# Performance work log

Hardware: AMD Instinct MI355X
Metric: run time of the kernel (lower is better)

The kernel has to match this reference:

```python
import jax, jax.numpy as jnp
import numpy as np

B, L, HIDDEN, HEAD_DIM = 8, 1024, 1024, 64


def setup_inputs() -> dict:
    key = jax.random.key(0)
    ks = jax.random.split(key, 11)
    s = 1.0 / np.sqrt(HIDDEN)
    return {
        "query": jax.random.normal(ks[0], (B, L, HIDDEN), jnp.float32),
        "key": jax.random.normal(ks[1], (B, L, HIDDEN), jnp.float32),
        "value": jax.random.normal(ks[2], (B, L, HIDDEN), jnp.float32),
        "k_bias_matrix": jax.random.normal(ks[3], (L, L, HEAD_DIM), jnp.float32) * 0.02,
        "v_bias_matrix": jax.random.normal(ks[4], (L, L, HEAD_DIM), jnp.float32) * 0.02,
        "Wq": jax.random.normal(ks[5], (HIDDEN, HEAD_DIM), jnp.float32) * s,
        "bq": jnp.zeros((HEAD_DIM,), jnp.float32),
        "Wk": jax.random.normal(ks[6], (HIDDEN, HEAD_DIM), jnp.float32) * s,
        "bk": jnp.zeros((HEAD_DIM,), jnp.float32),
        "Wv": jax.random.normal(ks[7], (HIDDEN, HEAD_DIM), jnp.float32) * s,
        "bv": jnp.zeros((HEAD_DIM,), jnp.float32),
        "mask": jnp.ones((B, L), jnp.int32),
    }


def reference(query, key, value, k_bias_matrix, v_bias_matrix, Wq, bq, Wk, bk, Wv, bv, mask):
    # projections to head_dim
    q = query @ Wq + bq  # [B,L,D]
    k = key @ Wk + bk    # [B,L,D]
    v = value @ Wv + bv  # [B,L,D]
    # content scores + relative key-bias scores (Shaw et al.)
    attn_1 = jnp.einsum('bqd,bkd->bqk', q, k)              # [B,L,L]
    attn_2 = jnp.einsum('bqd,qkd->bqk', q, k_bias_matrix)  # [B,L,L]
    scores = (attn_1 + attn_2) / jnp.sqrt(jnp.asarray(q.shape[-1], q.dtype))
    scores = jnp.where(mask[:, None, :] == 0, jnp.asarray(-1e9, scores.dtype), scores)
    w = jax.nn.softmax(scores, axis=-1)                    # [B,L,L]
    values_1 = jnp.einsum('bqk,bkd->bqd', w, v)
    values_2 = jnp.einsum('bqk,qkd->bqd', w, v_bias_matrix)
    return values_1 + values_2
```

## Files before the change

kernel.cpp:

```cpp
#include <hip/hip_runtime.h>

#define B_ 8
#define L_ 1024
#define HID_ 1024
#define D_ 64

typedef short bf16x8 __attribute__((ext_vector_type(8)));
typedef float f32x4 __attribute__((ext_vector_type(4)));

__device__ inline short f2bf(float f) {
    unsigned u = __builtin_bit_cast(unsigned, f);
    unsigned r = (u + 0x7fffu + ((u >> 16) & 1u)) >> 16;
    return (short)r;
}

__global__ __launch_bounds__(256) void proj_kernel(
    const float* __restrict__ query, const float* __restrict__ key, const float* __restrict__ value,
    const float* __restrict__ Wq, const float* __restrict__ bq,
    const float* __restrict__ Wk, const float* __restrict__ bk,
    const float* __restrict__ Wv, const float* __restrict__ bv,
    float* __restrict__ qp, float* __restrict__ kp, float* __restrict__ vp)
{
    const int which = blockIdx.y;
    const float* in   = which == 0 ? query : (which == 1 ? key : value);
    const float* W    = which == 0 ? Wq : (which == 1 ? Wk : Wv);
    const float* bias = which == 0 ? bq : (which == 1 ? bk : bv);
    float* out        = which == 0 ? qp : (which == 1 ? kp : vp);

    __shared__ float Xs[64][68];
    __shared__ float Ws[64][64];

    const int t  = threadIdx.x;
    const int tx = t & 15;
    const int ty = t >> 4;
    const int r0 = blockIdx.x * 64;

    float acc[4][4] = {};
    for (int kk = 0; kk < HID_; kk += 64) {
        {
            const int r  = t >> 4;
            const int c4 = t & 15;
            #pragma unroll
            for (int i = 0; i < 4; i++) {
                float4 x = *(const float4*)(in + (size_t)(r0 + r + 16 * i) * HID_ + kk + 4 * c4);
                *(float4*)(&Xs[r + 16 * i][4 * c4]) = x;
                float4 w = *(const float4*)(W + (size_t)(kk + r + 16 * i) * D_ + 4 * c4);
                *(float4*)(&Ws[r + 16 * i][4 * c4]) = w;
            }
        }
        __syncthreads();
        #pragma unroll 8
        for (int k = 0; k < 64; k++) {
            float4 b4 = *(const float4*)(&Ws[k][4 * tx]);
            #pragma unroll
            for (int i = 0; i < 4; i++) {
                float a = Xs[4 * ty + i][k];
                acc[i][0] += a * b4.x;
                acc[i][1] += a * b4.y;
                acc[i][2] += a * b4.z;
                acc[i][3] += a * b4.w;
            }
        }
        __syncthreads();
    }
    float4 bb = *(const float4*)(bias + 4 * tx);
    #pragma unroll
    for (int i = 0; i < 4; i++) {
        float4 o;
        o.x = acc[i][0] + bb.x; o.y = acc[i][1] + bb.y;
        o.z = acc[i][2] + bb.z; o.w = acc[i][3] + bb.w;
        *(float4*)(out + (size_t)(r0 + 4 * ty + i) * D_ + 4 * tx) = o;
    }
}

__global__ __launch_bounds__(256) void attn1_kernel(
    const float* __restrict__ qp, const float* __restrict__ kp,
    const int* __restrict__ mask, float* __restrict__ s1)
{
    const int b  = blockIdx.z;
    const int q0 = blockIdx.y * 128;
    const int k0 = blockIdx.x * 128;
    __shared__ float qs[128][68];
    __shared__ float ks[128][68];
    const int t = threadIdx.x;
    {
        const int row = t >> 4;
        const int c4  = t & 15;
        #pragma unroll
        for (int i = 0; i < 8; i++) {
            int r = row + 16 * i;
            *(float4*)&qs[r][c4 * 4] = *(const float4*)(qp + ((size_t)b * L_ + q0 + r) * D_ + c4 * 4);
            *(float4*)&ks[r][c4 * 4] = *(const float4*)(kp + ((size_t)b * L_ + k0 + r) * D_ + c4 * 4);
        }
    }
    __syncthreads();
    const int tx = t & 15, ty = t >> 4;
    float acc[8][8] = {};
    for (int d4 = 0; d4 < 16; d4++) {
        float4 qv[8], kv[8];
        #pragma unroll
        for (int i = 0; i < 8; i++) qv[i] = *(const float4*)&qs[ty + 16 * i][d4 * 4];
        #pragma unroll
        for (int j = 0; j < 8; j++) kv[j] = *(const float4*)&ks[tx + 16 * j][d4 * 4];
        #pragma unroll
        for (int i = 0; i < 8; i++)
            #pragma unroll
            for (int j = 0; j < 8; j++)
                acc[i][j] += qv[i].x * kv[j].x + qv[i].y * kv[j].y +
                             qv[i].z * kv[j].z + qv[i].w * kv[j].w;
    }
    #pragma unroll
    for (int j = 0; j < 8; j++) {
        int kg = k0 + tx + 16 * j;
        bool live = mask[b * L_ + kg] != 0;
        #pragma unroll
        for (int i = 0; i < 8; i++) {
            int qg = q0 + ty + 16 * i;
            s1[((size_t)b * L_ + qg) * L_ + kg] = live ? acc[i][j] * 0.125f : -1e9f;
        }
    }
}

#define KS_ 1032
__global__ __launch_bounds__(512) void row_kernel(
    const float* __restrict__ qp, const float* __restrict__ kb,
    const float* __restrict__ vb, float* __restrict__ s1w,
    float* __restrict__ out)
{
    __shared__ float sc[2 * 8 * KS_];
    __shared__ short qbf[2 * 16 * 64];
    const int t = threadIdx.x;
    const int wave = t >> 6, lane = t & 63;
    const int q0 = blockIdx.x * 2;

    #pragma unroll
    for (int i = 0; i < 4; i++) {
        int idx = t + 512 * i;
        int d = idx & 63, bq = idx >> 6;
        int b = bq & 15, q = bq >> 4;
        float v = (b < 8) ? 0.125f * qp[((size_t)b * L_ + q0 + q) * D_ + d] : 0.0f;
        qbf[idx] = f2bf(v);
    }
    __syncthreads();

    for (int job = wave; job < 128; job += 8) {
        int q = job >> 6, kt = job & 63;
        int k0 = kt * 16;
        const float* abase = kb + ((size_t)(q0 + q) * L_ + k0 + (lane & 15)) * D_ + (lane >> 4) * 8;
        f32x4 acc = {0.f, 0.f, 0.f, 0.f};
        #pragma unroll
        for (int h = 0; h < 2; h++) {
            float4 x0 = *(const float4*)(abase + h * 32);
            float4 x1 = *(const float4*)(abase + h * 32 + 4);
            bf16x8 a;
            a[0] = f2bf(x0.x); a[1] = f2bf(x0.y); a[2] = f2bf(x0.z); a[3] = f2bf(x0.w);
            a[4] = f2bf(x1.x); a[5] = f2bf(x1.y); a[6] = f2bf(x1.z); a[7] = f2bf(x1.w);
            bf16x8 bq = *(const bf16x8*)&qbf[(q * 16 + (lane & 15)) * 64 + h * 32 + (lane >> 4) * 8];
            acc = __builtin_amdgcn_mfma_f32_16x16x32_bf16(a, bq, acc, 0, 0, 0);
        }
        int b = lane & 15;
        if (b < 8) {
            float* dst = &sc[(q * 8 + b) * KS_ + k0 + (lane >> 4) * 4];
            dst[0] = acc[0]; dst[1] = acc[1]; dst[2] = acc[2]; dst[3] = acc[3];
        }
    }
    __syncthreads();

    #pragma unroll
    for (int i = 0; i < 8; i++) {
        int idx = t + 512 * i;
        int c4 = idx & 255;
        int row = idx >> 8;
        int b = row & 7, q = row >> 3;
        float4 s = *(const float4*)(s1w + ((size_t)b * L_ + q0 + q) * L_ + c4 * 4);
        float* dst = &sc[(q * 8 + b) * KS_ + c4 * 4];
        float4 cur = *(float4*)dst;
        cur.x += s.x; cur.y += s.y; cur.z += s.z; cur.w += s.w;
        *(float4*)dst = cur;
    }
    __syncthreads();

    for (int r = wave; r < 16; r += 8) {
        int q = r >> 3, b = r & 7;
        float* rowp = &sc[r * KS_];
        float* wrow = s1w + ((size_t)b * L_ + q0 + q) * L_;
        float4 x[4];
        float m = -1e30f;
        #pragma unroll
        for (int j = 0; j < 4; j++) {
            x[j] = *(const float4*)&rowp[lane * 4 + 256 * j];
            m = fmaxf(m, fmaxf(fmaxf(x[j].x, x[j].y), fmaxf(x[j].z, x[j].w)));
        }
        #pragma unroll
        for (int off = 32; off; off >>= 1) m = fmaxf(m, __shfl_xor(m, off));
        float s = 0.f;
        #pragma unroll
        for (int j = 0; j < 4; j++) {
            x[j].x = __expf(x[j].x - m); x[j].y = __expf(x[j].y - m);
            x[j].z = __expf(x[j].z - m); x[j].w = __expf(x[j].w - m);
            s += x[j].x + x[j].y + x[j].z + x[j].w;
        }
        #pragma unroll
        for (int off = 32; off; off >>= 1) s += __shfl_xor(s, off);
        float inv = 1.0f / s;
        #pragma unroll
        for (int j = 0; j < 4; j++) {
            x[j].x *= inv; x[j].y *= inv; x[j].z *= inv; x[j].w *= inv;
            *(float4*)&rowp[lane * 4 + 256 * j] = x[j];
            *(float4*)&wrow[lane * 4 + 256 * j] = x[j];
        }
    }
    __syncthreads();

    {
        const int q  = wave >> 2;
        const int kqi = wave & 3;
        const int kq = kqi * 256;
        const int kl = lane >> 4;
        const int d4 = lane & 15;
        float acc[8][4] = {};
        const float* vbbase = vb + ((size_t)(q0 + q) * L_ + kq + kl) * D_ + d4 * 4;
        #pragma unroll 4
        for (int j = 0; j < 64; j++) {
            int k = kq + j * 4 + kl;
            float4 vb4 = *(const float4*)(vbbase + (size_t)j * 4 * D_);
            #pragma unroll
            for (int b = 0; b < 8; b++) {
                float wgt = sc[(q * 8 + b) * KS_ + k];
                acc[b][0] += wgt * vb4.x;
                acc[b][1] += wgt * vb4.y;
                acc[b][2] += wgt * vb4.z;
                acc[b][3] += wgt * vb4.w;
            }
        }
        #pragma unroll
        for (int b = 0; b < 8; b++)
            #pragma unroll
            for (int j = 0; j < 4; j++) {
                float v = acc[b][j];
                v += __shfl_down(v, 32);
                v += __shfl_down(v, 16);
                acc[b][j] = v;
            }
        __syncthreads();
        float* part = sc;
        if (lane < 16) {
            #pragma unroll
            for (int b = 0; b < 8; b++) {
                float4 o; o.x = acc[b][0]; o.y = acc[b][1]; o.z = acc[b][2]; o.w = acc[b][3];
                *(float4*)&part[(((q * 4 + kqi) * 8) + b) * 64 + d4 * 4] = o;
            }
        }
        __syncthreads();
        for (int i = t; i < 1024; i += 512) {
            int d = i & 63; int bq = i >> 6; int b = bq & 7; int q2 = bq >> 3;
            float s = part[((q2 * 4 + 0) * 8 + b) * 64 + d] +
                      part[((q2 * 4 + 1) * 8 + b) * 64 + d] +
                      part[((q2 * 4 + 2) * 8 + b) * 64 + d] +
                      part[((q2 * 4 + 3) * 8 + b) * 64 + d];
            out[((size_t)b * L_ + q0 + q2) * D_ + d] = s;
        }
    }
}

__global__ __launch_bounds__(256) void pv_kernel(
    const float* __restrict__ w, const float* __restrict__ vp, float* __restrict__ out)
{
    const int b  = blockIdx.y;
    const int q0 = blockIdx.x * 16;
    __shared__ float ws_[16][68];
    __shared__ float vs[64][64];
    const int t  = threadIdx.x;
    const int tx = t & 15;
    const int ty = t >> 4;
    float acc[4] = {};
    for (int kk = 0; kk < L_; kk += 64) {
        {
            int qi = t >> 4, kc = t & 15;
            float4 x = *(const float4*)(w + ((size_t)b * L_ + q0 + qi) * L_ + kk + 4 * kc);
            *(float4*)(&ws_[qi][4 * kc]) = x;
        }
        #pragma unroll
        for (int i = 0; i < 4; i++) {
            int f4 = t + 256 * i;
            int kr = f4 >> 4, dc = f4 & 15;
            float4 x = *(const float4*)(vp + ((size_t)b * L_ + kk + kr) * D_ + 4 * dc);
            *(float4*)(&vs[kr][4 * dc]) = x;
        }
        __syncthreads();
        #pragma unroll 8
        for (int k = 0; k < 64; k++) {
            float4 v4 = *(const float4*)(&vs[k][4 * tx]);
            float a = ws_[ty][k];
            acc[0] += a * v4.x; acc[1] += a * v4.y;
            acc[2] += a * v4.z; acc[3] += a * v4.w;
        }
        __syncthreads();
    }
    float* dst = out + ((size_t)b * L_ + q0 + ty) * D_ + 4 * tx;
    float4 o = *(const float4*)dst;
    o.x += acc[0]; o.y += acc[1]; o.z += acc[2]; o.w += acc[3];
    *(float4*)dst = o;
}

extern "C" void kernel_launch(void* const* d_in, const int* in_sizes, int n_in,
                              void* d_out, int out_size, void* d_ws, size_t ws_size,
                              hipStream_t stream)
{
    const float* query = (const float*)d_in[0];
    const float* key   = (const float*)d_in[1];
    const float* value = (const float*)d_in[2];
    const float* kb    = (const float*)d_in[3];
    const float* vb    = (const float*)d_in[4];
    const float* Wq    = (const float*)d_in[5];
    const float* bq    = (const float*)d_in[6];
    const float* Wk    = (const float*)d_in[7];
    const float* bk    = (const float*)d_in[8];
    const float* Wv    = (const float*)d_in[9];
    const float* bv    = (const float*)d_in[10];
    const int*   mask  = (const int*)d_in[11];
    float* out = (float*)d_out;

    float* ws = (float*)d_ws;
    const size_t PROJ = (size_t)B_ * L_ * D_;
    float* qp = ws;
    float* kp = ws + PROJ;
    float* vp = ws + 2 * PROJ;
    float* s1 = ws + 3 * PROJ;

    proj_kernel<<<dim3(128, 3), 256, 0, stream>>>(query, key, value,
                                                  Wq, bq, Wk, bk, Wv, bv,
                                                  qp, kp, vp);
    attn1_kernel<<<dim3(8, 8, 8), 256, 0, stream>>>(qp, kp, mask, s1);
    row_kernel<<<512, 512, 0, stream>>>(qp, kb, vb, s1, out);
    pv_kernel<<<dim3(64, 8), 256, 0, stream>>>(s1, vp, out);
}
```

Measured before the change: 690.4 us.

## Move QKV projection onto bf16 MFMA with split hi/lo precision

Replaces the fp32 shared-memory FMA projection with MFMA 16x16x32 bf16 instructions. Each fp32 activation is split into bf16 hi and lo parts, and three MFMAs per tile approximate fp32 accuracy. The weights are pre-split and pre-swizzled into MFMA fragment layout by a new small kernel that runs every call. This drops the LDS staging and syncs in exchange for an extra launch and some per-element conversion work.

New measurement: 684.9 us. No clear change (-0.8%).

```diff
diff --git a/kernel.cpp b/kernel.cpp
--- a/kernel.cpp
+++ b/kernel.cpp
@@ -13,63 +13,87 @@
     unsigned r = (u + 0x7fffu + ((u >> 16) & 1u)) >> 16;
     return (short)r;
 }
+__device__ inline float bf2f(short h) {
+    unsigned u = ((unsigned)(unsigned short)h) << 16;
+    return __builtin_bit_cast(float, u);
+}
+
+__global__ __launch_bounds__(256) void wconv_kernel(
+    const float* __restrict__ Wq, const float* __restrict__ Wk, const float* __restrict__ Wv,
+    unsigned short* __restrict__ whi, unsigned short* __restrict__ wlo)
+{
+    int t = blockIdx.x * 256 + threadIdx.x;
+    int which = t >> 16;
+    int rem = t & 65535;
+    int j = rem & 7, lane = (rem >> 3) & 63, ks = (rem >> 9) & 31, n = rem >> 14;
+    int k = ks * 32 + (lane >> 4) * 8 + j;
+    int d = n * 16 + (lane & 15);
+    const float* W = which == 0 ? Wq : (which == 1 ? Wk : Wv);
+    float v = W[k * D_ + d];
+    short h = f2bf(v);
+    whi[t] = (unsigned short)h;
+    wlo[t] = (unsigned short)f2bf(v - bf2f(h));
+}
 
 __global__ __launch_bounds__(256) void proj_kernel(
     const float* __restrict__ query, const float* __restrict__ key, const float* __restrict__ value,
-    const float* __restrict__ Wq, const float* __restrict__ bq,
-    const float* __restrict__ Wk, const float* __restrict__ bk,
-    const float* __restrict__ Wv, const float* __restrict__ bv,
+    const float* __restrict__ bq, const float* __restrict__ bk, const float* __restrict__ bv,
+    const unsigned short* __restrict__ whi, const unsigned short* __restrict__ wlo,
     float* __restrict__ qp, float* __restrict__ kp, float* __restrict__ vp)
 {
-    const int which = blockIdx.y;
+    const int blk = blockIdx.x;
+    const int which = blk >> 7;
+    const int r0 = (blk & 127) * 64;
     const float* in   = which == 0 ? query : (which == 1 ? key : value);
-    const float* W    = which == 0 ? Wq : (which == 1 ? Wk : Wv);
     const float* bias = which == 0 ? bq : (which == 1 ? bk : bv);
     float* out        = which == 0 ? qp : (which == 1 ? kp : vp);
-
-    __shared__ float Xs[64][68];
-    __shared__ float Ws[64][64];
-
-    const int t  = threadIdx.x;
-    const int tx = t & 15;
-    const int ty = t >> 4;
-    const int r0 = blockIdx.x * 64;
-
-    float acc[4][4] = {};
-    for (int kk = 0; kk < HID_; kk += 64) {
+    const unsigned short* wh = whi + (size_t)which * 65536;
+    const unsigned short* wl = wlo + (size_t)which * 65536;
+
+    const int wave = threadIdx.x >> 6, lane = threadIdx.x & 63;
+    const int lr = lane & 15, lg = lane >> 4;
+
+    const float* arow = in + (size_t)(r0 + wave * 16 + lr) * HID_ + lg * 8;
+
+    f32x4 acc[4];
+    #pragma unroll
+    for (int n = 0; n < 4; n++) acc[n] = (f32x4){0.f, 0.f, 0.f, 0.f};
+
+    #pragma unroll 2
+    for (int ks = 0; ks < 32; ks++) {
+        float4 x0 = *(const float4*)(arow + ks * 32);
+        float4 x1 = *(const float4*)(arow + ks * 32 + 4);
+        bf16x8 ahi, alo;
         {
-            const int r  = t >> 4;
-            const int c4 = t & 15;
-            #pragma unroll
-            for (int i = 0; i < 4; i++) {
-                float4 x = *(const float4*)(in + (size_t)(r0 + r + 16 * i) * HID_ + kk + 4 * c4);
-                *(float4*)(&Xs[r + 16 * i][4 * c4]) = x;
-                float4 w = *(const float4*)(W + (size_t)(kk + r + 16 * i) * D_ + 4 * c4);
-                *(float4*)(&Ws[r + 16 * i][4 * c4]) = w;
-            }
-        }
-        __syncthreads();
-        #pragma unroll 8
-        for (int k = 0; k < 64; k++) {
-            float4 b4 = *(const float4*)(&Ws[k][4 * tx]);
-            #pragma unroll
-            for (int i = 0; i < 4; i++) {
-                float a = Xs[4 * ty + i][k];
-                acc[i][0] += a * b4.x;
-                acc[i][1] += a * b4.y;
-                acc[i][2] += a * b4.z;
-                acc[i][3] += a * b4.w;
-            }
-        }
-        __syncthreads();
-    }
-    float4 bb = *(const float4*)(bias + 4 * tx);
-    #pragma unroll
-    for (int i = 0; i < 4; i++) {
-        float4 o;
-        o.x = acc[i][0] + bb.x; o.y = acc[i][1] + bb.y;
-        o.z = acc[i][2] + bb.z; o.w = acc[i][3] + bb.w;
-        *(float4*)(out + (size_t)(r0 + 4 * ty + i) * D_ + 4 * tx) = o;
+            float xs0 = x0.x, xs1 = x0.y, xs2 = x0.z, xs3 = x0.w;
+            float xs4 = x1.x, xs5 = x1.y, xs6 = x1.z, xs7 = x1.w;
+            short h;
+            h = f2bf(xs0); ahi[0] = h; alo[0] = f2bf(xs0 - bf2f(h));
+            h = f2bf(xs1); ahi[1] = h; alo[1] = f2bf(xs1 - bf2f(h));
+            h = f2bf(xs2); ahi[2] = h; alo[2] = f2bf(xs2 - bf2f(h));
+            h = f2bf(xs3); ahi[3] = h; alo[3] = f2bf(xs3 - bf2f(h));
+            h = f2bf(xs4); ahi[4] = h; alo[4] = f2bf(xs4 - bf2f(h));
+            h = f2bf(xs5); ahi[5] = h; alo[5] = f2bf(xs5 - bf2f(h));
+            h = f2bf(xs6); ahi[6] = h; alo[6] = f2bf(xs6 - bf2f(h));
+            h = f2bf(xs7); ahi[7] = h; alo[7] = f2bf(xs7 - bf2f(h));
+        }
+        #pragma unroll
+        for (int n = 0; n < 4; n++) {
+            const size_t fo = ((size_t)(n * 32 + ks) * 64 + lane) * 8;
+            bf16x8 bhi = *(const bf16x8*)(wh + fo);
+            bf16x8 blo = *(const bf16x8*)(wl + fo);
+            acc[n] = __builtin_amdgcn_mfma_f32_16x16x32_bf16(ahi, bhi, acc[n], 0, 0, 0);
+            acc[n] = __builtin_amdgcn_mfma_f32_16x16x32_bf16(alo, bhi, acc[n], 0, 0, 0);
+            acc[n] = __builtin_amdgcn_mfma_f32_16x16x32_bf16(ahi, blo, acc[n], 0, 0, 0);
+        }
+    }
+    #pragma unroll
+    for (int n = 0; n < 4; n++) {
+        float bv_ = bias[n * 16 + lr];
+        #pragma unroll
+        for (int i = 0; i < 4; i++) {
+            out[(size_t)(r0 + wave * 16 + lg * 4 + i) * D_ + n * 16 + lr] = acc[n][i] + bv_;
+        }
     }
 }
 
@@ -327,10 +351,11 @@
     float* kp = ws + PROJ;
     float* vp = ws + 2 * PROJ;
     float* s1 = ws + 3 * PROJ;
-
-    proj_kernel<<<dim3(128, 3), 256, 0, stream>>>(query, key, value,
-                                                  Wq, bq, Wk, bk, Wv, bv,
-                                                  qp, kp, vp);
+    unsigned short* whi = (unsigned short*)(ws + 3 * PROJ + (size_t)B_ * L_ * L_);
+    unsigned short* wlo = whi + 3 * 65536;
+
+    wconv_kernel<<<768, 256, 0, stream>>>(Wq, Wk, Wv, whi, wlo);
+    proj_kernel<<<384, 256, 0, stream>>>(query, key, value, bq, bk, bv, whi, wlo, qp, kp, vp);
     attn1_kernel<<<dim3(8, 8, 8), 256, 0, stream>>>(qp, kp, mask, s1);
     row_kernel<<<512, 512, 0, stream>>>(qp, kb, vb, s1, out);
     pv_kernel<<<dim3(64, 8), 256, 0, stream>>>(s1, vp, out);
```
